# Kernel optimization log

Measured on AMD Instinct MI355X. Metric: run time of the kernel, lower is better.

Reference implementation:

```python
import jax, jax.numpy as jnp
import numpy as np
from jax import lax

B, C, T, S = 32, 122, 500, 13
WID, EMB, PROJ = 80, 8, 1024
HID = 768  # (H=1)*(W=96)*(E=8) after CNN
EPS = 1e-5
DN = ('NCHW', 'OIHW', 'NCHW')


def setup_inputs() -> dict:
    key = jax.random.key(0)
    ks = jax.random.split(key, 24)
    f32 = jnp.float32
    def n(k, shape, scale):
        return (jax.random.normal(k, shape, dtype=f32) * scale).astype(f32)
    return {
        'x': jax.random.normal(ks[0], (B, C, T), dtype=f32),
        'subject_ids': jax.random.randint(ks[1], (B,), 0, S, dtype=jnp.int32),
        'W_sub': n(ks[2], (S, T, T), 0.04),      # nn.Linear(500,500) weight per subject
        'b_sub': n(ks[3], (S, T), 0.02),
        'conv1_w': n(ks[4], (WID, 1, 1, 5), 0.3),
        'conv1_b': n(ks[5], (WID,), 0.02),
        'bn1_g': 1.0 + n(ks[6], (WID,), 0.1),
        'bn1_b': n(ks[7], (WID,), 0.1),
        'bn1_m': n(ks[8], (WID,), 0.1),
        'bn1_v': 0.5 + jax.random.uniform(ks[9], (WID,), dtype=f32),
        'conv2_w': n(ks[10], (WID, WID, C, 1), 0.01),
        'conv2_b': n(ks[11], (WID,), 0.02),
        'bn2_g': 1.0 + n(ks[12], (WID,), 0.1),
        'bn2_b': n(ks[13], (WID,), 0.1),
        'bn2_m': n(ks[14], (WID,), 0.1),
        'bn2_v': 0.5 + jax.random.uniform(ks[15], (WID,), dtype=f32),
        'proj_w': n(ks[16], (EMB, WID, 1, 1), 0.1),
        'proj_b': n(ks[17], (EMB,), 0.02),
        'mlp1_w': n(ks[18], (PROJ, HID), 0.03),
        'mlp1_b': n(ks[19], (PROJ,), 0.02),
        'mlp2_w': n(ks[20], (PROJ, PROJ), 0.03),
        'mlp2_b': n(ks[21], (PROJ,), 0.02),
        'ln_g': 1.0 + n(ks[22], (PROJ,), 0.05),
        'ln_b': n(ks[23], (PROJ,), 0.05),
    }


def _bn(h, g, b, m, v):
    # eval-mode BatchNorm2d over channel axis 1
    scale = (g / jnp.sqrt(v + EPS))[None, :, None, None]
    shift = (b - m * g / jnp.sqrt(v + EPS))[None, :, None, None]
    return h * scale + shift


def _forward(x, subject_ids, W_sub, b_sub, conv1_w, conv1_b, bn1_g, bn1_b, bn1_m, bn1_v,
             conv2_w, conv2_b, bn2_g, bn2_b, bn2_m, bn2_v, proj_w, proj_b,
             mlp1_w, mlp1_b, mlp2_w, mlp2_b, ln_g, ln_b):
    # --- per-subject routing: gather each sample's Linear(500,500) and apply ---
    Wg = W_sub[subject_ids]                       # [B,T,T] (out,in)
    bg = b_sub[subject_ids]                       # [B,T]
    out = jnp.einsum('bcs,bts->bct', x, Wg) + bg[:, None, :]
    # --- spatio-temporal CNN (eval mode: dropout = identity) ---
    h = out[:, None, :, :]                        # [B,1,C,T]
    h = lax.conv_general_dilated(h, conv1_w, (1, 1), 'VALID', dimension_numbers=DN)
    h = h + conv1_b[None, :, None, None]          # [B,80,122,496]
    h = lax.reduce_window(h, 0.0, lax.add, (1, 1, 1, 17), (1, 1, 1, 5), 'VALID') / 17.0  # [B,80,122,96]
    h = jax.nn.elu(_bn(h, bn1_g, bn1_b, bn1_m, bn1_v))
    h = lax.conv_general_dilated(h, conv2_w, (1, 1), 'VALID', dimension_numbers=DN)
    h = h + conv2_b[None, :, None, None]          # [B,80,1,96]
    h = jax.nn.elu(_bn(h, bn2_g, bn2_b, bn2_m, bn2_v))
    h = lax.conv_general_dilated(h, proj_w, (1, 1), 'VALID', dimension_numbers=DN)
    h = h + proj_b[None, :, None, None]           # [B,8,1,96]
    z = jnp.transpose(h, (0, 2, 3, 1)).reshape(h.shape[0], -1)  # [B,768]
    # --- MLP projector: Linear -> Residual(GELU+Linear) -> LayerNorm ---
    z1 = z @ mlp1_w.T + mlp1_b                    # [B,1024]
    r = jax.nn.gelu(z1, approximate=False) @ mlp2_w.T + mlp2_b
    y = z1 + r
    mu = jnp.mean(y, axis=-1, keepdims=True)
    var = jnp.var(y, axis=-1, keepdims=True)
    return (y - mu) / jnp.sqrt(var + EPS) * ln_g + ln_b


def reference(x, subject_ids, W_sub, b_sub, conv1_w, conv1_b, bn1_g, bn1_b, bn1_m, bn1_v,
              conv2_w, conv2_b, bn2_g, bn2_b, bn2_m, bn2_v, proj_w, proj_b,
              mlp1_w, mlp1_b, mlp2_w, mlp2_b, ln_g, ln_b):
    return _forward(x, subject_ids, W_sub, b_sub, conv1_w, conv1_b, bn1_g, bn1_b, bn1_m, bn1_v,
                    conv2_w, conv2_b, bn2_g, bn2_b, bn2_m, bn2_v, proj_w, proj_b,
                    mlp1_w, mlp1_b, mlp2_w, mlp2_b, ln_g, ln_b)
```

## Files before the change

### kernel.cpp

```cpp
#include <hip/hip_runtime.h>
#include <math.h>

#define BB 32
#define CC 122
#define TT 500
#define SS 13
#define WID 80
#define EMB 8
#define PROJ 1024
#define HID 768
#define TP 96
#define EPSF 1e-5f
#define KP 9760
#define KSPLIT 16

typedef float f32x4 __attribute__((ext_vector_type(4)));
typedef __bf16 bf16x8 __attribute__((ext_vector_type(8)));
typedef unsigned short u16x8 __attribute__((ext_vector_type(8)));
union BF8 { u16x8 u; bf16x8 b; };

__device__ __forceinline__ unsigned short f2bf(float f) {
    union { float f; unsigned u; } v; v.f = f;
    unsigned r = v.u + 0x7FFFu + ((v.u >> 16) & 1u);
    return (unsigned short)(r >> 16);
}

__device__ __forceinline__ float eluf(float x) {
    return x > 0.f ? x : __expf(x) - 1.f;
}

#define OFF_E    ((size_t)0)
#define OFF_XB   ((size_t)1952000)
#define OFF_WB   ((size_t)3000576)
#define OFF_W2P  ((size_t)4704512)
#define OFF_PART ((size_t)20086272)
#define OFF_Z    ((size_t)24018432)
#define OFF_Z1   ((size_t)24030720)
#define OFF_G    ((size_t)24063488)
#define OFF_Y    ((size_t)24079872)
#define OFF_W1B  ((size_t)24112640)
#define OFF_W2B  ((size_t)24505856)
#define OFF_WCB  ((size_t)25030144)
#define OFF_B1F  ((size_t)25031424)
#define OFF_SC2  ((size_t)25031504)
#define OFF_SH2  ((size_t)25031584)

#define NPK_X  (2097152)
#define NPK_W  (3407872)
#define NPK_W2 (780800)
#define NPK_M1 (786432)
#define NPK_M2 (1048576)
#define NPK_TOT (NPK_X + NPK_W + NPK_W2 + NPK_M1 + NPK_M2)

__global__ __launch_bounds__(256) void k_pack(const float* __restrict__ x,
                                              const float* __restrict__ W_sub,
                                              const float* __restrict__ conv2_w,
                                              const float* __restrict__ mlp1_w,
                                              const float* __restrict__ mlp2_w,
                                              const float* __restrict__ conv1_w, const float* __restrict__ conv1_b,
                                              const float* __restrict__ g1, const float* __restrict__ b1,
                                              const float* __restrict__ m1, const float* __restrict__ v1,
                                              const float* __restrict__ conv2_b, const float* __restrict__ g2,
                                              const float* __restrict__ b2, const float* __restrict__ m2,
                                              const float* __restrict__ v2,
                                              unsigned short* __restrict__ xb,
                                              unsigned short* __restrict__ wb,
                                              unsigned short* __restrict__ w2p,
                                              unsigned short* __restrict__ w1b,
                                              unsigned short* __restrict__ w2b,
                                              unsigned short* __restrict__ wcb, float* __restrict__ bias1f,
                                              float* __restrict__ scale2, float* __restrict__ shift2f) {
    if (blockIdx.x == 0) {
        int o = threadIdx.x;
        if (o < WID) {
            float s1 = g1[o] * rsqrtf(v1[o] + EPSF);
            float sh1 = b1[o] - m1[o] * s1;
            #pragma unroll
            for (int d = 0; d < 21; d++) {
                int klo = d - 16; if (klo < 0) klo = 0;
                int khi = d;      if (khi > 4) khi = 4;
                float acc = 0.f;
                for (int k = klo; k <= khi; k++) acc += conv1_w[o*5 + k];
                wcb[o*32 + d] = f2bf(acc * s1 * (1.f/17.f));
            }
            #pragma unroll
            for (int d = 21; d < 32; d++) wcb[o*32 + d] = 0;
            bias1f[o] = conv1_b[o] * s1 + sh1;
            float s2 = g2[o] * rsqrtf(v2[o] + EPSF);
            scale2[o] = s2;
            shift2f[o] = conv2_b[o] * s2 + (b2[o] - m2[o] * s2);
        }
    }
    size_t idx = (size_t)blockIdx.x * 256 + threadIdx.x;
    if (idx >= (size_t)NPK_TOT) return;
    if (idx < NPK_X) {
        int s = idx & 511, c = (idx >> 9) & 127, b = idx >> 16;
        float v = (c < CC && s < TT) ? x[((size_t)b * CC + c) * TT + s] : 0.f;
        xb[idx] = f2bf(v);
    } else if (idx < NPK_X + NPK_W) {
        size_t j = idx - NPK_X;
        int s = j & 511, t = (j >> 9) & 511, sub = j >> 18;
        float v = (t < TT && s < TT) ? W_sub[((size_t)sub * TT + t) * TT + s] : 0.f;
        wb[j] = f2bf(v);
    } else if (idx < NPK_X + NPK_W + NPK_W2) {
        size_t j = idx - NPK_X - NPK_W;
        int o  = (int)(j / (WID * CC));
        int r  = (int)(j % (WID * CC));
        int op = r / CC, c = r % CC;
        w2p[(size_t)o * KP + (size_t)c * WID + op] = f2bf(conv2_w[j]);
    } else if (idx < NPK_X + NPK_W + NPK_W2 + NPK_M1) {
        size_t j = idx - NPK_X - NPK_W - NPK_W2;
        w1b[j] = f2bf(mlp1_w[j]);
    } else {
        size_t j = idx - NPK_X - NPK_W - NPK_W2 - NPK_M1;
        w2b[j] = f2bf(mlp2_w[j]);
    }
}

__global__ __launch_bounds__(256) void k_einsum(const unsigned short* __restrict__ xb,
                                                const unsigned short* __restrict__ wb,
                                                const int* __restrict__ sid,
                                                const float* __restrict__ b_sub,
                                                float* __restrict__ oute) {
    int t0 = blockIdx.x * 32, b = blockIdx.y;
    int s = sid[b];
    int tid = threadIdx.x, w = tid >> 6, lr = tid & 15, lg = (tid >> 4) & 3;
    const unsigned short* A0 = xb + ((size_t)(b * 128 + w * 32 + lr)) * 512 + 8 * lg;
    const unsigned short* Bb = wb + (size_t)s * 262144 + 8 * lg;
    f32x4 acc[2][2] = {};
    for (int kb = 0; kb < 512; kb += 32) {
        BF8 a0, a1;
        a0.u = *(const u16x8*)(A0 + kb);
        a1.u = *(const u16x8*)(A0 + 16 * 512 + kb);
        #pragma unroll
        for (int nt = 0; nt < 2; nt++) {
            BF8 bf; bf.u = *(const u16x8*)(Bb + (size_t)(t0 + nt * 16 + lr) * 512 + kb);
            acc[0][nt] = __builtin_amdgcn_mfma_f32_16x16x32_bf16(a0.b, bf.b, acc[0][nt], 0, 0, 0);
            acc[1][nt] = __builtin_amdgcn_mfma_f32_16x16x32_bf16(a1.b, bf.b, acc[1][nt], 0, 0, 0);
        }
    }
    const float* bg = b_sub + (size_t)s * TT;
    #pragma unroll
    for (int nt = 0; nt < 2; nt++) {
        int t = t0 + nt * 16 + lr;
        if (t < TT) {
            float bias = bg[t];
            #pragma unroll
            for (int mt = 0; mt < 2; mt++) {
                int crow = w * 32 + mt * 16 + 4 * lg;
                #pragma unroll
                for (int r = 0; r < 4; r++) {
                    int c = crow + r;
                    if (c < CC) oute[((size_t)b * CC + c) * TT + t] = acc[mt][nt][r] + bias;
                }
            }
        }
    }
}

__global__ __launch_bounds__(384) void k_fc(const float* __restrict__ oute,
                                            const unsigned short* __restrict__ wcb,
                                            const float* __restrict__ b1f,
                                            const unsigned short* __restrict__ w2p,
                                            float* __restrict__ part) {
    __shared__ float e2[2][512];
    __shared__ unsigned short pt[96][164];
    int chunk = blockIdx.x, b = blockIdx.y;
    int tid = threadIdx.x, w = tid >> 6, l = tid & 63, lr = l & 15, lg = l >> 4;
    BF8 af[5]; float4 bf4[5];
    #pragma unroll
    for (int ot = 0; ot < 5; ot++) {
        af[ot].u = *(const u16x8*)(wcb + (ot * 16 + lr) * 32 + 8 * lg);
        bf4[ot] = *(const float4*)(b1f + ot * 16 + 4 * lg);
    }
    const unsigned short* Arow = w2p + (size_t)lr * KP + 8 * lg;
    f32x4 acc2[5] = {};
    for (int ci = 0; ci < 4; ci++) {
        int cp = chunk * 4 + ci;
        bool live = cp < 61;
        if (live) {
            if (tid < 250) {
                int cc = tid / 125, i = tid % 125;
                ((float4*)e2[cc])[i] = ((const float4*)(oute + ((size_t)b * CC + cp * 2 + cc) * TT))[i];
            }
            if (tid >= 232 && tid < 256) {
                int j = tid - 232; int cc = j / 12, i = 500 + (j % 12);
                e2[cc][i] = 0.f;
            }
        }
        __syncthreads();
        if (live) {
            #pragma unroll
            for (int cc = 0; cc < 2; cc++) {
                int t = w * 16 + lr;
                const float* ew = e2[cc] + 5 * t + 8 * lg;
                BF8 bfr;
                #pragma unroll
                for (int j = 0; j < 8; j++) bfr.u[j] = f2bf(ew[j]);
                f32x4 fa[5] = {};
                #pragma unroll
                for (int ot = 0; ot < 5; ot++)
                    fa[ot] = __builtin_amdgcn_mfma_f32_16x16x32_bf16(af[ot].b, bfr.b, fa[ot], 0, 0, 0);
                #pragma unroll
                for (int ot = 0; ot < 5; ot++) {
                    union { unsigned short s[4]; uint2 v; } pk;
                    #pragma unroll
                    for (int r = 0; r < 4; r++) pk.s[r] = f2bf(eluf(fa[ot][r] + bf4[ot][r]));
                    *(uint2*)&pt[t][cc * 80 + ot * 16 + 4 * lg] = pk.v;
                }
            }
        }
        __syncthreads();
        if (live) {
            #pragma unroll
            for (int kl = 0; kl < 5; kl++) {
                BF8 bf; bf.u = *(const u16x8*)(&pt[w * 16 + lr][kl * 32 + lg * 8]);
                int ko = cp * 160 + kl * 32;
                #pragma unroll
                for (int mt = 0; mt < 5; mt++) {
                    BF8 a; a.u = *(const u16x8*)(Arow + (size_t)mt * 16 * KP + ko);
                    acc2[mt] = __builtin_amdgcn_mfma_f32_16x16x32_bf16(a.b, bf.b, acc2[mt], 0, 0, 0);
                }
            }
        }
    }
    float* pp = part + ((size_t)(chunk * BB + b) * WID) * TP;
    int t = w * 16 + lr;
    #pragma unroll
    for (int mt = 0; mt < 5; mt++) {
        int ob = mt * 16 + 4 * lg;
        #pragma unroll
        for (int r = 0; r < 4; r++)
            pp[(size_t)(ob + r) * TP + t] = acc2[mt][r];
    }
}

__global__ __launch_bounds__(256) void k_redproj(const float* __restrict__ part,
                                                 const float* __restrict__ scale2,
                                                 const float* __restrict__ shift2f,
                                                 const float* __restrict__ pw,
                                                 const float* __restrict__ pb,
                                                 unsigned short* __restrict__ zbf) {
    __shared__ float ly[WID * 12];
    __shared__ float lw[EMB * WID];
    int tq = blockIdx.x, b = blockIdx.y;
    int tid = threadIdx.x;
    int t0 = tq * 12;
    for (int i = tid; i < EMB * WID; i += 256) lw[i] = pw[i];
    if (tid < 240) {
        int o = tid / 3, q = tid % 3;
        const float* pbase = part + (size_t)b * (WID * TP) + o * TP + t0 + 4 * q;
        float4 a = {0.f, 0.f, 0.f, 0.f};
        #pragma unroll
        for (int ks = 0; ks < KSPLIT; ks++) {
            float4 v = *(const float4*)(pbase + (size_t)ks * (BB * WID * TP));
            a.x += v.x; a.y += v.y; a.z += v.z; a.w += v.w;
        }
        float sc = scale2[o], sh = shift2f[o];
        ly[o * 12 + 4 * q + 0] = eluf(a.x * sc + sh);
        ly[o * 12 + 4 * q + 1] = eluf(a.y * sc + sh);
        ly[o * 12 + 4 * q + 2] = eluf(a.z * sc + sh);
        ly[o * 12 + 4 * q + 3] = eluf(a.w * sc + sh);
    }
    __syncthreads();
    if (tid < 12 * EMB) {
        int e = tid & 7, tl = tid >> 3;
        float acc = pb[e];
        #pragma unroll 10
        for (int o = 0; o < WID; o++) acc = fmaf(ly[o * 12 + tl], lw[e * WID + o], acc);
        zbf[(size_t)b * HID + (t0 + tl) * EMB + e] = f2bf(acc);
    }
}

__global__ __launch_bounds__(256) void k_mlp1(const unsigned short* __restrict__ zbf,
                                              const unsigned short* __restrict__ w1b,
                                              const float* __restrict__ bias,
                                              float* __restrict__ z1,
                                              unsigned short* __restrict__ gbf) {
    __shared__ float accb[4][64][4];
    int cu = blockIdx.x >> 1, rh = blockIdx.x & 1;
    int tid = threadIdx.x, w = tid >> 6, l = tid & 63, lr = l & 15, lg = l >> 4;
    int pcol = cu * 16 + lr;
    const unsigned short* wr = w1b + (size_t)pcol * HID + w * 192 + 8 * lg;
    const unsigned short* za = zbf + (size_t)(rh * 16 + lr) * HID + w * 192 + 8 * lg;
    f32x4 acc = {};
    #pragma unroll
    for (int kb = 0; kb < 192; kb += 32) {
        BF8 bf; bf.u = *(const u16x8*)(wr + kb);
        BF8 a;  a.u  = *(const u16x8*)(za + kb);
        acc = __builtin_amdgcn_mfma_f32_16x16x32_bf16(a.b, bf.b, acc, 0, 0, 0);
    }
    #pragma unroll
    for (int r = 0; r < 4; r++) accb[w][l][r] = acc[r];
    __syncthreads();
    if (w == 0) {
        float bs = bias[pcol];
        #pragma unroll
        for (int r = 0; r < 4; r++) {
            int row = rh * 16 + 4 * lg + r;
            float v = bs;
            #pragma unroll
            for (int q = 0; q < 4; q++) v += accb[q][l][r];
            z1[(size_t)row * PROJ + pcol] = v;
            gbf[(size_t)row * PROJ + pcol] = f2bf(0.5f * v * (1.f + erff(v * 0.70710678118654752f)));
        }
    }
}

__global__ __launch_bounds__(256) void k_mlp2(const unsigned short* __restrict__ gbf,
                                              const float* __restrict__ z1,
                                              const unsigned short* __restrict__ w2b,
                                              const float* __restrict__ bias,
                                              float* __restrict__ y) {
    __shared__ float accb[4][64][4];
    int cu = blockIdx.x >> 1, rh = blockIdx.x & 1;
    int tid = threadIdx.x, w = tid >> 6, l = tid & 63, lr = l & 15, lg = l >> 4;
    int pc = cu * 16 + lr;
    const unsigned short* wr = w2b + (size_t)pc * PROJ + w * 256 + 8 * lg;
    const unsigned short* ga = gbf + (size_t)(rh * 16 + lr) * PROJ + w * 256 + 8 * lg;
    f32x4 acc = {};
    #pragma unroll
    for (int kb = 0; kb < 256; kb += 32) {
        BF8 bf; bf.u = *(const u16x8*)(wr + kb);
        BF8 a;  a.u  = *(const u16x8*)(ga + kb);
        acc = __builtin_amdgcn_mfma_f32_16x16x32_bf16(a.b, bf.b, acc, 0, 0, 0);
    }
    #pragma unroll
    for (int r = 0; r < 4; r++) accb[w][l][r] = acc[r];
    __syncthreads();
    if (w == 0) {
        float bs = bias[pc];
        #pragma unroll
        for (int r = 0; r < 4; r++) {
            int row = rh * 16 + 4 * lg + r;
            float v = bs + z1[(size_t)row * PROJ + pc];
            #pragma unroll
            for (int q = 0; q < 4; q++) v += accb[q][l][r];
            y[(size_t)row * PROJ + pc] = v;
        }
    }
}

__global__ __launch_bounds__(256) void k_ln(const float* __restrict__ y,
                                            const float* __restrict__ lg,
                                            const float* __restrict__ lb,
                                            float* __restrict__ out) {
    int b = blockIdx.x, tid = threadIdx.x;
    const float4* yr = (const float4*)(y + (size_t)b * PROJ);
    float4 v = yr[tid];
    float s  = v.x + v.y + v.z + v.w;
    float sq = v.x*v.x + v.y*v.y + v.z*v.z + v.w*v.w;
    #pragma unroll
    for (int off = 32; off > 0; off >>= 1) {
        s  += __shfl_down(s, off);
        sq += __shfl_down(sq, off);
    }
    __shared__ float ss[4], ssq[4];
    int wv = tid >> 6, lane = tid & 63;
    if (lane == 0) { ss[wv] = s; ssq[wv] = sq; }
    __syncthreads();
    __shared__ float smu, sinv;
    if (tid == 0) {
        float Sm = ss[0] + ss[1] + ss[2] + ss[3];
        float Sq = ssq[0] + ssq[1] + ssq[2] + ssq[3];
        float mu = Sm * (1.f / PROJ);
        float var = Sq * (1.f / PROJ) - mu * mu;
        smu = mu;
        sinv = rsqrtf(var + EPSF);
    }
    __syncthreads();
    float mu = smu, inv = sinv;
    float4 g4 = ((const float4*)lg)[tid];
    float4 b4 = ((const float4*)lb)[tid];
    float4 o4;
    o4.x = (v.x - mu) * inv * g4.x + b4.x;
    o4.y = (v.y - mu) * inv * g4.y + b4.y;
    o4.z = (v.z - mu) * inv * g4.z + b4.z;
    o4.w = (v.w - mu) * inv * g4.w + b4.w;
    ((float4*)(out + (size_t)b * PROJ))[tid] = o4;
}

extern "C" void kernel_launch(void* const* d_in, const int* in_sizes, int n_in,
                              void* d_out, int out_size, void* d_ws, size_t ws_size,
                              hipStream_t stream) {
    const float* x        = (const float*)d_in[0];
    const int*   sid      = (const int*)  d_in[1];
    const float* W_sub    = (const float*)d_in[2];
    const float* b_sub    = (const float*)d_in[3];
    const float* conv1_w  = (const float*)d_in[4];
    const float* conv1_b  = (const float*)d_in[5];
    const float* bn1_g    = (const float*)d_in[6];
    const float* bn1_b    = (const float*)d_in[7];
    const float* bn1_m    = (const float*)d_in[8];
    const float* bn1_v    = (const float*)d_in[9];
    const float* conv2_w  = (const float*)d_in[10];
    const float* conv2_b  = (const float*)d_in[11];
    const float* bn2_g    = (const float*)d_in[12];
    const float* bn2_b    = (const float*)d_in[13];
    const float* bn2_m    = (const float*)d_in[14];
    const float* bn2_v    = (const float*)d_in[15];
    const float* proj_w   = (const float*)d_in[16];
    const float* proj_b   = (const float*)d_in[17];
    const float* mlp1_w   = (const float*)d_in[18];
    const float* mlp1_b   = (const float*)d_in[19];
    const float* mlp2_w   = (const float*)d_in[20];
    const float* mlp2_b   = (const float*)d_in[21];
    const float* ln_g     = (const float*)d_in[22];
    const float* ln_b     = (const float*)d_in[23];
    float* out = (float*)d_out;
    float* ws  = (float*)d_ws;

    float* ws_e    = ws + OFF_E;
    unsigned short* ws_xb  = (unsigned short*)(ws + OFF_XB);
    unsigned short* ws_wb  = (unsigned short*)(ws + OFF_WB);
    unsigned short* ws_w2p = (unsigned short*)(ws + OFF_W2P);
    float* ws_part = ws + OFF_PART;
    unsigned short* ws_zbf = (unsigned short*)(ws + OFF_Z);
    float* ws_z1   = ws + OFF_Z1;
    unsigned short* ws_gbf = (unsigned short*)(ws + OFF_G);
    float* ws_y    = ws + OFF_Y;
    unsigned short* ws_w1b = (unsigned short*)(ws + OFF_W1B);
    unsigned short* ws_w2b = (unsigned short*)(ws + OFF_W2B);
    unsigned short* ws_wcb = (unsigned short*)(ws + OFF_WCB);
    float* ws_b1f  = ws + OFF_B1F;
    float* ws_sc2  = ws + OFF_SC2;
    float* ws_sh2  = ws + OFF_SH2;

    hipLaunchKernelGGL(k_pack, dim3((NPK_TOT + 255) / 256), dim3(256), 0, stream,
                       x, W_sub, conv2_w, mlp1_w, mlp2_w,
                       conv1_w, conv1_b, bn1_g, bn1_b, bn1_m, bn1_v,
                       conv2_b, bn2_g, bn2_b, bn2_m, bn2_v,
                       ws_xb, ws_wb, ws_w2p, ws_w1b, ws_w2b,
                       ws_wcb, ws_b1f, ws_sc2, ws_sh2);

    hipLaunchKernelGGL(k_einsum, dim3(16, BB), dim3(256), 0, stream,
                       ws_xb, ws_wb, sid, b_sub, ws_e);

    hipLaunchKernelGGL(k_fc, dim3(KSPLIT, BB), dim3(384), 0, stream,
                       ws_e, ws_wcb, ws_b1f, ws_w2p, ws_part);

    hipLaunchKernelGGL(k_redproj, dim3(8, BB), dim3(256), 0, stream,
                       ws_part, ws_sc2, ws_sh2, proj_w, proj_b, ws_zbf);

    hipLaunchKernelGGL(k_mlp1, dim3(128), dim3(256), 0, stream,
                       ws_zbf, ws_w1b, mlp1_b, ws_z1, ws_gbf);

    hipLaunchKernelGGL(k_mlp2, dim3(128), dim3(256), 0, stream,
                       ws_gbf, ws_z1, ws_w2b, mlp2_b, ws_y);

    hipLaunchKernelGGL(k_ln, dim3(BB), dim3(256), 0, stream,
                       ws_y, ln_g, ln_b, out);
}
```

Measured before the change: 200.7 us.

## Stage einsum weight tile in LDS and fuse MLP2 with LayerNorm

The subject-weight tile for each einsum block is copied into padded shared memory once, and the MFMA loop reads B fragments from there instead of global memory. The second MLP linear layer and the LayerNorm are merged into one kernel with one block per sample, which computes the dot products with scalar FMAs over bf16 weights and normalizes in place. This removes a launch and the intermediate y buffer. The trade-off is that every block rereads the full mlp2 weight matrix with strided per-thread row access, no MFMA, and only 32 blocks.

```diff
diff --git a/kernel.cpp b/kernel.cpp
--- a/kernel.cpp
+++ b/kernel.cpp
@@ -23,6 +23,11 @@
     union { float f; unsigned u; } v; v.f = f;
     unsigned r = v.u + 0x7FFFu + ((v.u >> 16) & 1u);
     return (unsigned short)(r >> 16);
+}
+
+__device__ __forceinline__ float bf2f(unsigned short u) {
+    union { unsigned u; float f; } v; v.u = (unsigned)u << 16;
+    return v.f;
 }
 
 __device__ __forceinline__ float eluf(float x) {
@@ -122,11 +127,20 @@
                                                 const int* __restrict__ sid,
                                                 const float* __restrict__ b_sub,
                                                 float* __restrict__ oute) {
+    __shared__ unsigned short bt[32 * 520];
     int t0 = blockIdx.x * 32, b = blockIdx.y;
     int s = sid[b];
     int tid = threadIdx.x, w = tid >> 6, lr = tid & 15, lg = (tid >> 4) & 3;
+    {
+        const unsigned short* src = wb + (size_t)s * 262144 + (size_t)t0 * 512;
+        #pragma unroll
+        for (int i = tid; i < 2048; i += 256) {
+            int row = i >> 6, col8 = i & 63;
+            *(u16x8*)(bt + row * 520 + col8 * 8) = *(const u16x8*)(src + row * 512 + col8 * 8);
+        }
+    }
+    __syncthreads();
     const unsigned short* A0 = xb + ((size_t)(b * 128 + w * 32 + lr)) * 512 + 8 * lg;
-    const unsigned short* Bb = wb + (size_t)s * 262144 + 8 * lg;
     f32x4 acc[2][2] = {};
     for (int kb = 0; kb < 512; kb += 32) {
         BF8 a0, a1;
@@ -134,7 +148,7 @@
         a1.u = *(const u16x8*)(A0 + 16 * 512 + kb);
         #pragma unroll
         for (int nt = 0; nt < 2; nt++) {
-            BF8 bf; bf.u = *(const u16x8*)(Bb + (size_t)(t0 + nt * 16 + lr) * 512 + kb);
+            BF8 bf; bf.u = *(const u16x8*)(bt + (nt * 16 + lr) * 520 + kb + 8 * lg);
             acc[0][nt] = __builtin_amdgcn_mfma_f32_16x16x32_bf16(a0.b, bf.b, acc[0][nt], 0, 0, 0);
             acc[1][nt] = __builtin_amdgcn_mfma_f32_16x16x32_bf16(a1.b, bf.b, acc[1][nt], 0, 0, 0);
         }
@@ -307,62 +321,53 @@
     }
 }
 
-__global__ __launch_bounds__(256) void k_mlp2(const unsigned short* __restrict__ gbf,
+__global__ __launch_bounds__(512) void k_m2ln(const unsigned short* __restrict__ gbf,
                                               const float* __restrict__ z1,
                                               const unsigned short* __restrict__ w2b,
                                               const float* __restrict__ bias,
-                                              float* __restrict__ y) {
-    __shared__ float accb[4][64][4];
-    int cu = blockIdx.x >> 1, rh = blockIdx.x & 1;
-    int tid = threadIdx.x, w = tid >> 6, l = tid & 63, lr = l & 15, lg = l >> 4;
-    int pc = cu * 16 + lr;
-    const unsigned short* wr = w2b + (size_t)pc * PROJ + w * 256 + 8 * lg;
-    const unsigned short* ga = gbf + (size_t)(rh * 16 + lr) * PROJ + w * 256 + 8 * lg;
-    f32x4 acc = {};
-    #pragma unroll
-    for (int kb = 0; kb < 256; kb += 32) {
-        BF8 bf; bf.u = *(const u16x8*)(wr + kb);
-        BF8 a;  a.u  = *(const u16x8*)(ga + kb);
-        acc = __builtin_amdgcn_mfma_f32_16x16x32_bf16(a.b, bf.b, acc, 0, 0, 0);
-    }
-    #pragma unroll
-    for (int r = 0; r < 4; r++) accb[w][l][r] = acc[r];
-    __syncthreads();
-    if (w == 0) {
-        float bs = bias[pc];
-        #pragma unroll
-        for (int r = 0; r < 4; r++) {
-            int row = rh * 16 + 4 * lg + r;
-            float v = bs + z1[(size_t)row * PROJ + pc];
-            #pragma unroll
-            for (int q = 0; q < 4; q++) v += accb[q][l][r];
-            y[(size_t)row * PROJ + pc] = v;
-        }
-    }
-}
-
-__global__ __launch_bounds__(256) void k_ln(const float* __restrict__ y,
-                                            const float* __restrict__ lg,
-                                            const float* __restrict__ lb,
-                                            float* __restrict__ out) {
+                                              const float* __restrict__ lngw,
+                                              const float* __restrict__ lnbw,
+                                              float* __restrict__ out) {
+    __shared__ float gv[PROJ];
+    __shared__ float ss[8], ssq[8];
+    __shared__ float smu, sinv;
     int b = blockIdx.x, tid = threadIdx.x;
-    const float4* yr = (const float4*)(y + (size_t)b * PROJ);
-    float4 v = yr[tid];
-    float s  = v.x + v.y + v.z + v.w;
-    float sq = v.x*v.x + v.y*v.y + v.z*v.z + v.w*v.w;
+    if (tid < 128) {
+        u16x8 g = *(const u16x8*)(gbf + (size_t)b * PROJ + tid * 8);
+        #pragma unroll
+        for (int j = 0; j < 8; j++) gv[tid * 8 + j] = bf2f(g[j]);
+    }
+    __syncthreads();
+    int q1 = tid, q2 = tid + 512;
+    const unsigned short* wr1 = w2b + (size_t)q1 * PROJ;
+    const unsigned short* wr2 = w2b + (size_t)q2 * PROJ;
+    float acc1 = 0.f, acc2 = 0.f;
+    #pragma unroll 4
+    for (int k = 0; k < PROJ; k += 8) {
+        u16x8 wa = *(const u16x8*)(wr1 + k);
+        u16x8 wc = *(const u16x8*)(wr2 + k);
+        const float* g = gv + k;
+        #pragma unroll
+        for (int j = 0; j < 8; j++) {
+            acc1 = fmaf(bf2f(wa[j]), g[j], acc1);
+            acc2 = fmaf(bf2f(wc[j]), g[j], acc2);
+        }
+    }
+    float y1 = acc1 + bias[q1] + z1[(size_t)b * PROJ + q1];
+    float y2 = acc2 + bias[q2] + z1[(size_t)b * PROJ + q2];
+    float s = y1 + y2, sq = y1 * y1 + y2 * y2;
     #pragma unroll
     for (int off = 32; off > 0; off >>= 1) {
         s  += __shfl_down(s, off);
         sq += __shfl_down(sq, off);
     }
-    __shared__ float ss[4], ssq[4];
     int wv = tid >> 6, lane = tid & 63;
     if (lane == 0) { ss[wv] = s; ssq[wv] = sq; }
     __syncthreads();
-    __shared__ float smu, sinv;
     if (tid == 0) {
-        float Sm = ss[0] + ss[1] + ss[2] + ss[3];
-        float Sq = ssq[0] + ssq[1] + ssq[2] + ssq[3];
+        float Sm = 0.f, Sq = 0.f;
+        #pragma unroll
+        for (int q = 0; q < 8; q++) { Sm += ss[q]; Sq += ssq[q]; }
         float mu = Sm * (1.f / PROJ);
         float var = Sq * (1.f / PROJ) - mu * mu;
         smu = mu;
@@ -370,14 +375,8 @@
     }
     __syncthreads();
     float mu = smu, inv = sinv;
-    float4 g4 = ((const float4*)lg)[tid];
-    float4 b4 = ((const float4*)lb)[tid];
-    float4 o4;
-    o4.x = (v.x - mu) * inv * g4.x + b4.x;
-    o4.y = (v.y - mu) * inv * g4.y + b4.y;
-    o4.z = (v.z - mu) * inv * g4.z + b4.z;
-    o4.w = (v.w - mu) * inv * g4.w + b4.w;
-    ((float4*)(out + (size_t)b * PROJ))[tid] = o4;
+    out[(size_t)b * PROJ + q1] = (y1 - mu) * inv * lngw[q1] + lnbw[q1];
+    out[(size_t)b * PROJ + q2] = (y2 - mu) * inv * lngw[q2] + lnbw[q2];
 }
 
 extern "C" void kernel_launch(void* const* d_in, const int* in_sizes, int n_in,
@@ -418,7 +417,6 @@
     unsigned short* ws_zbf = (unsigned short*)(ws + OFF_Z);
     float* ws_z1   = ws + OFF_Z1;
     unsigned short* ws_gbf = (unsigned short*)(ws + OFF_G);
-    float* ws_y    = ws + OFF_Y;
     unsigned short* ws_w1b = (unsigned short*)(ws + OFF_W1B);
     unsigned short* ws_w2b = (unsigned short*)(ws + OFF_W2B);
     unsigned short* ws_wcb = (unsigned short*)(ws + OFF_WCB);
@@ -445,9 +443,6 @@
     hipLaunchKernelGGL(k_mlp1, dim3(128), dim3(256), 0, stream,
                        ws_zbf, ws_w1b, mlp1_b, ws_z1, ws_gbf);
 
-    hipLaunchKernelGGL(k_mlp2, dim3(128), dim3(256), 0, stream,
-                       ws_gbf, ws_z1, ws_w2b, mlp2_b, ws_y);
-
-    hipLaunchKernelGGL(k_ln, dim3(BB), dim3(256), 0, stream,
-                       ws_y, ln_g, ln_b, out);
-}
+    hipLaunchKernelGGL(k_m2ln, dim3(BB), dim3(512), 0, stream,
+                       ws_gbf, ws_z1, ws_w2b, mlp2_b, ln_g, ln_b, out);
+}
```

Result: slower. 248.9 us (+24.0%).

## Convert subject weights to bf16 inside einsum and store einsum output as bf16

Applied to the files above, without the earlier changes.

The pack kernel no longer converts all 13 subject matrices to bf16. Instead, each einsum block loads its 32-row slice of the selected subject's fp32 weights, converts it, and stages it in LDS as the MFMA B operand. The einsum output is now written as bf16, which halves the intermediate traffic, and k_fc reads bf16 directly without converting. The cost is that each batch sample re-reads and re-converts its subject's weights, plus an LDS staging step.

```diff
diff --git a/kernel.cpp b/kernel.cpp
--- a/kernel.cpp
+++ b/kernel.cpp
@@ -31,7 +31,6 @@
 
 #define OFF_E    ((size_t)0)
 #define OFF_XB   ((size_t)1952000)
-#define OFF_WB   ((size_t)3000576)
 #define OFF_W2P  ((size_t)4704512)
 #define OFF_PART ((size_t)20086272)
 #define OFF_Z    ((size_t)24018432)
@@ -46,14 +45,12 @@
 #define OFF_SH2  ((size_t)25031584)
 
 #define NPK_X  (2097152)
-#define NPK_W  (3407872)
 #define NPK_W2 (780800)
 #define NPK_M1 (786432)
 #define NPK_M2 (1048576)
-#define NPK_TOT (NPK_X + NPK_W + NPK_W2 + NPK_M1 + NPK_M2)
+#define NPK_TOT (NPK_X + NPK_W2 + NPK_M1 + NPK_M2)
 
 __global__ __launch_bounds__(256) void k_pack(const float* __restrict__ x,
-                                              const float* __restrict__ W_sub,
                                               const float* __restrict__ conv2_w,
                                               const float* __restrict__ mlp1_w,
                                               const float* __restrict__ mlp2_w,
@@ -64,7 +61,6 @@
                                               const float* __restrict__ b2, const float* __restrict__ m2,
                                               const float* __restrict__ v2,
                                               unsigned short* __restrict__ xb,
-                                              unsigned short* __restrict__ wb,
                                               unsigned short* __restrict__ w2p,
                                               unsigned short* __restrict__ w1b,
                                               unsigned short* __restrict__ w2b,
@@ -97,36 +93,56 @@
         int s = idx & 511, c = (idx >> 9) & 127, b = idx >> 16;
         float v = (c < CC && s < TT) ? x[((size_t)b * CC + c) * TT + s] : 0.f;
         xb[idx] = f2bf(v);
-    } else if (idx < NPK_X + NPK_W) {
+    } else if (idx < NPK_X + NPK_W2) {
         size_t j = idx - NPK_X;
-        int s = j & 511, t = (j >> 9) & 511, sub = j >> 18;
-        float v = (t < TT && s < TT) ? W_sub[((size_t)sub * TT + t) * TT + s] : 0.f;
-        wb[j] = f2bf(v);
-    } else if (idx < NPK_X + NPK_W + NPK_W2) {
-        size_t j = idx - NPK_X - NPK_W;
         int o  = (int)(j / (WID * CC));
         int r  = (int)(j % (WID * CC));
         int op = r / CC, c = r % CC;
         w2p[(size_t)o * KP + (size_t)c * WID + op] = f2bf(conv2_w[j]);
-    } else if (idx < NPK_X + NPK_W + NPK_W2 + NPK_M1) {
-        size_t j = idx - NPK_X - NPK_W - NPK_W2;
+    } else if (idx < NPK_X + NPK_W2 + NPK_M1) {
+        size_t j = idx - NPK_X - NPK_W2;
         w1b[j] = f2bf(mlp1_w[j]);
     } else {
-        size_t j = idx - NPK_X - NPK_W - NPK_W2 - NPK_M1;
+        size_t j = idx - NPK_X - NPK_W2 - NPK_M1;
         w2b[j] = f2bf(mlp2_w[j]);
     }
 }
 
 __global__ __launch_bounds__(256) void k_einsum(const unsigned short* __restrict__ xb,
-                                                const unsigned short* __restrict__ wb,
+                                                const float* __restrict__ W_sub,
                                                 const int* __restrict__ sid,
                                                 const float* __restrict__ b_sub,
-                                                float* __restrict__ oute) {
+                                                unsigned short* __restrict__ oute) {
+    __shared__ unsigned short bt[32 * 520];
     int t0 = blockIdx.x * 32, b = blockIdx.y;
     int s = sid[b];
     int tid = threadIdx.x, w = tid >> 6, lr = tid & 15, lg = (tid >> 4) & 3;
+    {
+        const float* src = W_sub + (size_t)s * (TT * TT);
+        for (int i = tid; i < 2048; i += 256) {
+            int row = i >> 6;
+            int c0  = (i & 63) << 3;
+            int rt  = t0 + row;
+            union { unsigned short h[8]; uint4 q; } pk;
+            if (rt < TT && c0 + 8 <= TT) {
+                const float* p = src + (size_t)rt * TT + c0;
+                float4 v0 = *(const float4*)p;
+                float4 v1 = *(const float4*)(p + 4);
+                pk.h[0] = f2bf(v0.x); pk.h[1] = f2bf(v0.y);
+                pk.h[2] = f2bf(v0.z); pk.h[3] = f2bf(v0.w);
+                pk.h[4] = f2bf(v1.x); pk.h[5] = f2bf(v1.y);
+                pk.h[6] = f2bf(v1.z); pk.h[7] = f2bf(v1.w);
+            } else {
+                const float* p = src + (size_t)rt * TT;
+                #pragma unroll
+                for (int j = 0; j < 8; j++)
+                    pk.h[j] = (rt < TT && c0 + j < TT) ? f2bf(p[c0 + j]) : (unsigned short)0;
+            }
+            *(uint4*)(&bt[row * 520 + c0]) = pk.q;
+        }
+    }
+    __syncthreads();
     const unsigned short* A0 = xb + ((size_t)(b * 128 + w * 32 + lr)) * 512 + 8 * lg;
-    const unsigned short* Bb = wb + (size_t)s * 262144 + 8 * lg;
     f32x4 acc[2][2] = {};
     for (int kb = 0; kb < 512; kb += 32) {
         BF8 a0, a1;
@@ -134,7 +150,7 @@
         a1.u = *(const u16x8*)(A0 + 16 * 512 + kb);
         #pragma unroll
         for (int nt = 0; nt < 2; nt++) {
-            BF8 bf; bf.u = *(const u16x8*)(Bb + (size_t)(t0 + nt * 16 + lr) * 512 + kb);
+            BF8 bf; bf.u = *(const u16x8*)(bt + (nt * 16 + lr) * 520 + kb + 8 * lg);
             acc[0][nt] = __builtin_amdgcn_mfma_f32_16x16x32_bf16(a0.b, bf.b, acc[0][nt], 0, 0, 0);
             acc[1][nt] = __builtin_amdgcn_mfma_f32_16x16x32_bf16(a1.b, bf.b, acc[1][nt], 0, 0, 0);
         }
@@ -151,19 +167,19 @@
                 #pragma unroll
                 for (int r = 0; r < 4; r++) {
                     int c = crow + r;
-                    if (c < CC) oute[((size_t)b * CC + c) * TT + t] = acc[mt][nt][r] + bias;
+                    if (c < CC) oute[((size_t)b * CC + c) * TT + t] = f2bf(acc[mt][nt][r] + bias);
                 }
             }
         }
     }
 }
 
-__global__ __launch_bounds__(384) void k_fc(const float* __restrict__ oute,
+__global__ __launch_bounds__(384) void k_fc(const unsigned short* __restrict__ oute,
                                             const unsigned short* __restrict__ wcb,
                                             const float* __restrict__ b1f,
                                             const unsigned short* __restrict__ w2p,
                                             float* __restrict__ part) {
-    __shared__ float e2[2][512];
+    __shared__ unsigned short e2[2][512];
     __shared__ unsigned short pt[96][164];
     int chunk = blockIdx.x, b = blockIdx.y;
     int tid = threadIdx.x, w = tid >> 6, l = tid & 63, lr = l & 15, lg = l >> 4;
@@ -181,11 +197,11 @@
         if (live) {
             if (tid < 250) {
                 int cc = tid / 125, i = tid % 125;
-                ((float4*)e2[cc])[i] = ((const float4*)(oute + ((size_t)b * CC + cp * 2 + cc) * TT))[i];
+                ((uint2*)e2[cc])[i] = ((const uint2*)(oute + ((size_t)b * CC + cp * 2 + cc) * TT))[i];
             }
             if (tid >= 232 && tid < 256) {
                 int j = tid - 232; int cc = j / 12, i = 500 + (j % 12);
-                e2[cc][i] = 0.f;
+                e2[cc][i] = 0;
             }
         }
         __syncthreads();
@@ -193,10 +209,10 @@
             #pragma unroll
             for (int cc = 0; cc < 2; cc++) {
                 int t = w * 16 + lr;
-                const float* ew = e2[cc] + 5 * t + 8 * lg;
+                const unsigned short* ew = e2[cc] + 5 * t + 8 * lg;
                 BF8 bfr;
                 #pragma unroll
-                for (int j = 0; j < 8; j++) bfr.u[j] = f2bf(ew[j]);
+                for (int j = 0; j < 8; j++) bfr.u[j] = ew[j];
                 f32x4 fa[5] = {};
                 #pragma unroll
                 for (int ot = 0; ot < 5; ot++)
@@ -410,9 +426,8 @@
     float* out = (float*)d_out;
     float* ws  = (float*)d_ws;
 
-    float* ws_e    = ws + OFF_E;
+    unsigned short* ws_e   = (unsigned short*)(ws + OFF_E);
     unsigned short* ws_xb  = (unsigned short*)(ws + OFF_XB);
-    unsigned short* ws_wb  = (unsigned short*)(ws + OFF_WB);
     unsigned short* ws_w2p = (unsigned short*)(ws + OFF_W2P);
     float* ws_part = ws + OFF_PART;
     unsigned short* ws_zbf = (unsigned short*)(ws + OFF_Z);
@@ -427,14 +442,14 @@
     float* ws_sh2  = ws + OFF_SH2;
 
     hipLaunchKernelGGL(k_pack, dim3((NPK_TOT + 255) / 256), dim3(256), 0, stream,
-                       x, W_sub, conv2_w, mlp1_w, mlp2_w,
+                       x, conv2_w, mlp1_w, mlp2_w,
                        conv1_w, conv1_b, bn1_g, bn1_b, bn1_m, bn1_v,
                        conv2_b, bn2_g, bn2_b, bn2_m, bn2_v,
-                       ws_xb, ws_wb, ws_w2p, ws_w1b, ws_w2b,
+                       ws_xb, ws_w2p, ws_w1b, ws_w2b,
                        ws_wcb, ws_b1f, ws_sc2, ws_sh2);
 
     hipLaunchKernelGGL(k_einsum, dim3(16, BB), dim3(256), 0, stream,
-                       ws_xb, ws_wb, sid, b_sub, ws_e);
+                       ws_xb, W_sub, sid, b_sub, ws_e);
 
     hipLaunchKernelGGL(k_fc, dim3(KSPLIT, BB), dim3(384), 0, stream,
                        ws_e, ws_wcb, ws_b1f, ws_w2p, ws_part);
```

Measured after the change: 199.3 us. Within noise of the previous version (-0.7%).
